# Kernel optimization log

Measured on AMD Instinct MI355X. Metric: run time of the kernel, lower is better.

## Reference

```python
import jax, jax.numpy as jnp
import numpy as np

N = 100000   # nodes
E = 1600000  # edges (avg degree 16)
D = 256      # in_channels == dim (forward hard-codes BatchNorm1d(256))
BN_EPS = 1e-5


def _batchnorm(x, gamma, beta):
    # training-mode BatchNorm1d: batch statistics over node dim, biased variance
    mu = jnp.mean(x, axis=0)
    var = jnp.var(x, axis=0)
    return (x - mu) * jax.lax.rsqrt(var + BN_EPS) * gamma + beta


def _gin_conv(x, src, dst, n, W1, b1, gamma, beta, W2, b2):
    # GINConv, eps=0: nn((1+eps)*x + sum_{j in N(i)} x_j)
    agg = jax.ops.segment_sum(x[src], dst, num_segments=n)  # sparse neighbor sum
    h = x + agg
    h = jax.nn.relu(_batchnorm(h @ W1 + b1, gamma, beta))
    return jax.nn.relu(h @ W2 + b2)


def setup_inputs() -> dict:
    key = jax.random.key(0)
    ks = jax.random.split(key, 8)
    x = jax.random.normal(ks[0], (N, D), dtype=jnp.float32)
    edge_index = jax.random.randint(ks[1], (2, E), 0, N, dtype=jnp.int64)
    s = 0.02
    inp = {
        "x": x,
        "edge_index": edge_index,
        # fresh BatchNorm1d(256) in forward (default affine params)
        "g0": jnp.ones((D,), jnp.float32),
        "b0": jnp.zeros((D,), jnp.float32),
        # conv1 MLP: Linear-BN-ReLU-Linear-ReLU
        "W1a": jax.random.normal(ks[2], (D, D), jnp.float32) * s,
        "b1a": jnp.zeros((D,), jnp.float32),
        "g1": jnp.ones((D,), jnp.float32),
        "bt1": jnp.zeros((D,), jnp.float32),
        "W1b": jax.random.normal(ks[3], (D, D), jnp.float32) * s,
        "b1b": jnp.zeros((D,), jnp.float32),
        # conv2 MLP
        "W2a": jax.random.normal(ks[4], (D, D), jnp.float32) * s,
        "b2a": jnp.zeros((D,), jnp.float32),
        "g2": jnp.ones((D,), jnp.float32),
        "bt2": jnp.zeros((D,), jnp.float32),
        "W2b": jax.random.normal(ks[5], (D, D), jnp.float32) * s,
        "b2b": jnp.zeros((D,), jnp.float32),
    }
    return inp


def reference(x, edge_index, g0, b0, W1a, b1a, g1, bt1, W1b, b1b,
              W2a, b2a, g2, bt2, W2b, b2b):
    n = x.shape[0]
    src, dst = edge_index[0], edge_index[1]
    h = _batchnorm(x, g0, b0)                       # fresh BN(256) on input
    h = _gin_conv(h, src, dst, n, W1a, b1a, g1, bt1, W1b, b1b)
    h = jax.nn.relu(h)                              # outer relu (dropout=eval, identity)
    h = _gin_conv(h, src, dst, n, W2a, b2a, g2, bt2, W2b, b2b)
    return jax.nn.relu(h)
```

## Files before the change

kernel.cpp:

```cpp
#include <hip/hip_runtime.h>

#define N_NODES 100000
#define N_EDGES 1600000
#define DIM 256
#define NBINS 196
#define BINCAP 16384

typedef unsigned short bf16u;
typedef __attribute__((ext_vector_type(8))) short bf16x8s;
typedef __attribute__((ext_vector_type(4))) float f32x4;

__device__ __forceinline__ float bf2f(unsigned int u16) {
    union { unsigned int i; float f; } x; x.i = u16 << 16; return x.f;
}
__device__ __forceinline__ float hi2f(unsigned int u) {
    union { unsigned int i; float f; } x; x.i = u & 0xffff0000u; return x.f;
}
__device__ __forceinline__ float lo2f(unsigned int u) {
    union { unsigned int i; float f; } x; x.i = u << 16; return x.f;
}
__device__ __forceinline__ bf16u f2bf(float f) {
    union { float f; unsigned int i; } x; x.f = f;
    unsigned int i = x.i;
    return (bf16u)((i + 0x7fffu + ((i >> 16) & 1u)) >> 16);
}
__device__ __forceinline__ float loadv(const void* p, size_t i, int isf32) {
    return isf32 ? ((const float*)p)[i] : bf2f(((const bf16u*)p)[i]);
}
__device__ __forceinline__ void async_copy16(const void* g, void* l) {
    __builtin_amdgcn_global_load_lds((const __attribute__((address_space(1))) void*)g,
                                     (__attribute__((address_space(3))) void*)l, 16, 0, 0);
}

__global__ void zero_floats(float* p, int n) {
    int i = blockIdx.x * 256 + threadIdx.x;
    if (i < n) p[i] = 0.f;
}

__global__ void detect_flags(const unsigned* xw, const int* ei, int* flags, int* gBinFill) {
    __shared__ int cnt, nz;
    if (threadIdx.x == 0) { cnt = 0; nz = 0; }
    __syncthreads();
    gBinFill[threadIdx.x] = 0;
    unsigned u = xw[threadIdx.x];
    float av = fabsf(bf2f(u & 0xffffu));
    if (av > 1e-5f && av < 50.f) atomicAdd(&cnt, 1);
    if (ei[2 * threadIdx.x + 1] != 0) atomicAdd(&nz, 1);
    __syncthreads();
    if (threadIdx.x == 0) {
        flags[0] = (cnt >= 128) ? 0 : 1;
        if (nz == 0) { flags[1] = 2; flags[2] = 2 * N_EDGES; }
        else         { flags[1] = 1; flags[2] = N_EDGES; }
    }
}

__global__ void transpose_w(const void* W0, const void* W1, const void* W2, const void* W3,
                            bf16u* Wt, const int* flags) {
    __shared__ bf16u tile[64][65];
    int isf32 = flags[0];
    const void* W = (blockIdx.y == 0) ? W0 : (blockIdx.y == 1) ? W1 : (blockIdx.y == 2) ? W2 : W3;
    bf16u* out = Wt + (size_t)blockIdx.y * DIM * DIM;
    int t = threadIdx.x;
    int tx = t & 63, ty = t >> 6;
    int k0 = (blockIdx.x >> 2) * 64, n0 = (blockIdx.x & 3) * 64;
#pragma unroll
    for (int i = 0; i < 16; ++i) {
        int r = ty + i * 4;
        tile[tx][r] = f2bf(loadv(W, (size_t)(k0 + r) * DIM + (n0 + tx), isf32));
    }
    __syncthreads();
#pragma unroll
    for (int i = 0; i < 16; ++i) {
        int r = ty + i * 4;
        out[(size_t)(n0 + r) * DIM + (k0 + tx)] = tile[r][tx];
    }
}

__global__ __launch_bounds__(256) void bin_scatter(const int* __restrict__ ei,
                                                   const int* __restrict__ flags,
                                                   uint2* __restrict__ gRec,
                                                   int* __restrict__ gBinFill) {
    __shared__ int cnt[256];
    __shared__ int cur[256];
    __shared__ uint2 rec[4096];
    int t = threadIdx.x;
    cnt[t] = 0; cur[t] = 0;
    __syncthreads();
    int st = flags[1], ofs = flags[2];
    int e0 = blockIdx.x * 4096;
#pragma unroll
    for (int i = 0; i < 16; ++i) {
        int e = e0 + i * 256 + t;
        uint2 r;
        if (e < N_EDGES) {
            r.x = (unsigned)ei[(size_t)ofs + (size_t)e * st];
            r.y = (unsigned)ei[(size_t)e * st];
            atomicAdd(&cnt[r.x >> 9], 1);
        } else {
            r.x = 0xffffffffu; r.y = 0;
        }
        rec[i * 256 + t] = r;
    }
    __syncthreads();
    if (t < NBINS) {
        int c = cnt[t];
        int b = (c > 0) ? atomicAdd(&gBinFill[t], c) : 0;
        cnt[t] = b;
    }
    __syncthreads();
#pragma unroll
    for (int i = 0; i < 16; ++i) {
        uint2 r = rec[i * 256 + t];
        if (r.x != 0xffffffffu) {
            int b = r.x >> 9;
            int li = atomicAdd(&cur[b], 1);
            int pos = cnt[b] + li;
            if (pos < BINCAP) gRec[(size_t)b * BINCAP + pos] = r;
        }
    }
}

__global__ void bin_scan(const int* gBinFill, int* binBase) {
    __shared__ int s[256];
    int t = threadIdx.x;
    s[t] = (t < NBINS) ? gBinFill[t] : 0;
    __syncthreads();
    for (int off = 1; off < 256; off <<= 1) {
        int v = (t >= off) ? s[t - off] : 0;
        __syncthreads();
        s[t] += v;
        __syncthreads();
    }
    binBase[t + 1] = s[t];
    if (t == 0) binBase[0] = 0;
}

__global__ __launch_bounds__(256) void bin_csr(const uint2* __restrict__ gRec,
                                               const int* __restrict__ gBinFill,
                                               const int* __restrict__ binBase,
                                               int* __restrict__ rp, int* __restrict__ col) {
    __shared__ int cntA[512], scanB[512], noff[512], ncur[512];
    int bin = blockIdx.x, t = threadIdx.x;
    int cnt = gBinFill[bin];
    if (cnt > BINCAP) cnt = BINCAP;
    int gbase = binBase[bin], lo = bin << 9;
    cntA[t] = 0; cntA[t + 256] = 0; ncur[t] = 0; ncur[t + 256] = 0;
    __syncthreads();
    const uint2* R = gRec + (size_t)bin * BINCAP;
    for (int j = t; j < cnt; j += 256) atomicAdd(&cntA[(int)R[j].x - lo], 1);
    __syncthreads();
    scanB[t] = cntA[t]; scanB[t + 256] = cntA[t + 256];
    __syncthreads();
    for (int off = 1; off < 512; off <<= 1) {
        int v0 = (t >= off) ? scanB[t - off] : 0;
        int v1 = (t + 256 >= off) ? scanB[t + 256 - off] : 0;
        __syncthreads();
        scanB[t] += v0; scanB[t + 256] += v1;
        __syncthreads();
    }
    noff[t] = scanB[t] - cntA[t];
    noff[t + 256] = scanB[t + 256] - cntA[t + 256];
    __syncthreads();
    int n0 = lo + t, n1 = lo + t + 256;
    if (n0 < N_NODES) rp[n0] = gbase + noff[t];
    if (n1 < N_NODES) rp[n1] = gbase + noff[t + 256];
    if (bin == 0 && t == 0) rp[N_NODES] = N_EDGES;
    for (int j = t; j < cnt; j += 256) {
        uint2 r = R[j];
        int k = (int)r.x - lo;
        int li = atomicAdd(&ncur[k], 1);
        col[gbase + noff[k] + li] = (int)r.y;
    }
}

__global__ void col_stats(const void* X, int nrows, float* sums, const int* flags, int dual) {
    __shared__ float ls[512];
    int isf32 = dual ? flags[0] : 0;
    int t = threadIdx.x;
    ls[t] = 0.f; ls[t + 256] = 0.f;
    __syncthreads();
    int rpb = (nrows + gridDim.x - 1) / gridDim.x;
    int r0 = blockIdx.x * rpb;
    int r1 = r0 + rpb; if (r1 > nrows) r1 = nrows;
    int cg = (t & 31) * 8;
    float s[8], q[8];
#pragma unroll
    for (int j = 0; j < 8; ++j) { s[j] = 0.f; q[j] = 0.f; }
    for (int r = r0 + (t >> 5); r < r1; r += 8) {
        size_t base = (size_t)r * DIM + cg;
#pragma unroll
        for (int j = 0; j < 8; ++j) {
            float f = loadv(X, base + j, isf32);
            s[j] += f; q[j] += f * f;
        }
    }
#pragma unroll
    for (int j = 0; j < 8; ++j) {
        atomicAdd(&ls[cg + j], s[j]);
        atomicAdd(&ls[256 + cg + j], q[j]);
    }
    __syncthreads();
    atomicAdd(&sums[t], ls[t]);
    atomicAdd(&sums[256 + t], ls[256 + t]);
}

__global__ void bn_finalize(const float* sums, const void* gamma, const void* beta,
                            float* sc, float* sh, float inv_n, const int* flags) {
    int isf32 = flags[0];
    int t = threadIdx.x;
    float mu = sums[t] * inv_n;
    float var = sums[256 + t] * inv_n - mu * mu;
    float rs = rsqrtf(var + 1e-5f);
    float g = loadv(gamma, t, isf32), b = loadv(beta, t, isf32);
    sc[t] = rs * g;
    sh[t] = b - mu * rs * g;
}

__global__ void bn_apply(const void* X, const float* sc, const float* sh, bf16u* Y,
                         const int* flags, int dual, int relu) {
    int isf32 = dual ? flags[0] : 0;
    size_t i = (size_t)blockIdx.x * 256 + threadIdx.x;
    int c = ((int)(i & 31)) * 8;
    size_t base = i * 8;
    float v[8];
    if (isf32) {
        f32x4 x0 = *(const f32x4*)((const float*)X + base);
        f32x4 x1 = *(const f32x4*)((const float*)X + base + 4);
#pragma unroll
        for (int j = 0; j < 4; ++j) { v[j] = x0[j]; v[4 + j] = x1[j]; }
    } else {
        uint4 u = *(const uint4*)((const bf16u*)X + base);
        v[0] = lo2f(u.x); v[1] = hi2f(u.x);
        v[2] = lo2f(u.y); v[3] = hi2f(u.y);
        v[4] = lo2f(u.z); v[5] = hi2f(u.z);
        v[6] = lo2f(u.w); v[7] = hi2f(u.w);
    }
    f32x4 s0 = *(const f32x4*)(sc + c), s1 = *(const f32x4*)(sc + c + 4);
    f32x4 h0 = *(const f32x4*)(sh + c), h1 = *(const f32x4*)(sh + c + 4);
    float y[8];
#pragma unroll
    for (int j = 0; j < 4; ++j) {
        y[j]     = v[j]     * s0[j] + h0[j];
        y[4 + j] = v[4 + j] * s1[j] + h1[j];
    }
    if (relu) {
#pragma unroll
        for (int j = 0; j < 8; ++j) y[j] = fmaxf(y[j], 0.f);
    }
    uint4 ov;
    ov.x = (unsigned)f2bf(y[0]) | ((unsigned)f2bf(y[1]) << 16);
    ov.y = (unsigned)f2bf(y[2]) | ((unsigned)f2bf(y[3]) << 16);
    ov.z = (unsigned)f2bf(y[4]) | ((unsigned)f2bf(y[5]) << 16);
    ov.w = (unsigned)f2bf(y[6]) | ((unsigned)f2bf(y[7]) << 16);
    *(uint4*)(Y + base) = ov;
}

__global__ __launch_bounds__(256) void aggregate(const bf16u* __restrict__ h,
                                                 const int* __restrict__ rp,
                                                 const int* __restrict__ col,
                                                 bf16u* __restrict__ out) {
    int node = blockIdx.x * 4 + (threadIdx.x >> 6);
    int lane = threadIdx.x & 63;
    int p = lane >> 5, c = lane & 31;
    const uint4* hv = (const uint4*)h;
    float acc[8];
    if (p == 0) {
        uint4 u = hv[(size_t)node * 32 + c];
        acc[0] = lo2f(u.x); acc[1] = hi2f(u.x);
        acc[2] = lo2f(u.y); acc[3] = hi2f(u.y);
        acc[4] = lo2f(u.z); acc[5] = hi2f(u.z);
        acc[6] = lo2f(u.w); acc[7] = hi2f(u.w);
    } else {
#pragma unroll
        for (int j = 0; j < 8; ++j) acc[j] = 0.f;
    }
    int e = rp[node], e1 = rp[node + 1];
    for (; e + 4 <= e1; e += 4) {
        int s0 = col[e + p];
        int s1 = col[e + 2 + p];
        uint4 a = hv[(size_t)s0 * 32 + c];
        uint4 b = hv[(size_t)s1 * 32 + c];
        acc[0] += lo2f(a.x); acc[1] += hi2f(a.x);
        acc[2] += lo2f(a.y); acc[3] += hi2f(a.y);
        acc[4] += lo2f(a.z); acc[5] += hi2f(a.z);
        acc[6] += lo2f(a.w); acc[7] += hi2f(a.w);
        acc[0] += lo2f(b.x); acc[1] += hi2f(b.x);
        acc[2] += lo2f(b.y); acc[3] += hi2f(b.y);
        acc[4] += lo2f(b.z); acc[5] += hi2f(b.z);
        acc[6] += lo2f(b.w); acc[7] += hi2f(b.w);
    }
    for (; e < e1; e += 2) {
        int idx = e + p;
        if (idx < e1) {
            uint4 a = hv[(size_t)col[idx] * 32 + c];
            acc[0] += lo2f(a.x); acc[1] += hi2f(a.x);
            acc[2] += lo2f(a.y); acc[3] += hi2f(a.y);
            acc[4] += lo2f(a.z); acc[5] += hi2f(a.z);
            acc[6] += lo2f(a.w); acc[7] += hi2f(a.w);
        }
    }
#pragma unroll
    for (int j = 0; j < 8; ++j) acc[j] += __shfl_xor(acc[j], 32);
    if (p == 0) {
        uint4 ov;
        ov.x = (unsigned)f2bf(acc[0]) | ((unsigned)f2bf(acc[1]) << 16);
        ov.y = (unsigned)f2bf(acc[2]) | ((unsigned)f2bf(acc[3]) << 16);
        ov.z = (unsigned)f2bf(acc[4]) | ((unsigned)f2bf(acc[5]) << 16);
        ov.w = (unsigned)f2bf(acc[6]) | ((unsigned)f2bf(acc[7]) << 16);
        ((uint4*)out)[(size_t)node * 32 + c] = ov;
    }
}

__global__ __launch_bounds__(256) void gemm_bias(const bf16u* __restrict__ A,
                                                 const bf16u* __restrict__ Wt,
                                                 const void* __restrict__ bias,
                                                 void* __restrict__ Cout, int mrows,
                                                 const int* __restrict__ flags,
                                                 int relu, int f32out,
                                                 float* __restrict__ stats) {
    __shared__ bf16u As[128 * 64];
    __shared__ bf16u Bs[128 * 64];
    __shared__ float lsum[256];
    int isf32 = flags[0];
    int t = threadIdx.x;
    int w = t >> 6, lane = t & 63;
    int lr = lane & 15, lq = lane >> 4;
    int wm = w >> 1, wn = w & 1;
    int rowBase = blockIdx.x * 128, colBase = blockIdx.y * 128;
    f32x4 acc[4][4] = {};
    lsum[t] = 0.f;
    int srow = t >> 3;
    int g8   = ((t & 7) ^ ((t >> 3) & 7)) * 8;
    for (int k0 = 0; k0 < 256; k0 += 64) {
        __syncthreads();
#pragma unroll
        for (int p = 0; p < 4; ++p) {
            int r = p * 32 + srow;
            int gr = rowBase + r; gr = (gr < mrows) ? gr : (mrows - 1);
            async_copy16(A + (size_t)gr * 256 + k0 + g8, &As[(p * 32 + (w << 3)) * 64]);
            async_copy16(Wt + (size_t)(colBase + r) * 256 + k0 + g8, &Bs[(p * 32 + (w << 3)) * 64]);
        }
        __syncthreads();
#pragma unroll
        for (int ks = 0; ks < 2; ++ks) {
            bf16x8s af[4], bfv[4];
#pragma unroll
            for (int mt = 0; mt < 4; ++mt) {
                int ar = wm * 64 + mt * 16 + lr;
                af[mt] = *(const bf16x8s*)&As[ar * 64 + (((ks * 4 + lq) ^ (lr & 7)) * 8)];
            }
#pragma unroll
            for (int nt = 0; nt < 4; ++nt) {
                int br = wn * 64 + nt * 16 + lr;
                bfv[nt] = *(const bf16x8s*)&Bs[br * 64 + (((ks * 4 + lq) ^ (lr & 7)) * 8)];
            }
#pragma unroll
            for (int mt = 0; mt < 4; ++mt)
#pragma unroll
                for (int nt = 0; nt < 4; ++nt)
                    acc[mt][nt] = __builtin_amdgcn_mfma_f32_16x16x32_bf16(af[mt], bfv[nt], acc[mt][nt], 0, 0, 0);
        }
    }
    int storef32 = f32out && isf32;
#pragma unroll
    for (int nt = 0; nt < 4; ++nt) {
        int cl = wn * 64 + nt * 16 + lr;
        int c = colBase + cl;
        float bv = loadv(bias, c, isf32);
        float ssum = 0.f, ssq = 0.f;
#pragma unroll
        for (int mt = 0; mt < 4; ++mt) {
            int r0 = rowBase + wm * 64 + mt * 16 + lq * 4;
#pragma unroll
            for (int j = 0; j < 4; ++j) {
                int r = r0 + j;
                if (r < mrows) {
                    float y = acc[mt][nt][j] + bv;
                    if (relu) y = fmaxf(y, 0.f);
                    if (storef32) ((float*)Cout)[(size_t)r * 256 + c] = y;
                    else          ((bf16u*)Cout)[(size_t)r * 256 + c] = f2bf(y);
                    ssum += y; ssq += y * y;
                }
            }
        }
        if (stats) {
            atomicAdd(&lsum[cl], ssum);
            atomicAdd(&lsum[128 + cl], ssq);
        }
    }
    if (stats) {
        __syncthreads();
        if (t < 128) {
            atomicAdd(&stats[colBase + t], lsum[t]);
            atomicAdd(&stats[256 + colBase + t], lsum[128 + t]);
        }
    }
}

extern "C" void kernel_launch(void* const* d_in, const int* in_sizes, int n_in,
                              void* d_out, int out_size, void* d_ws, size_t ws_size,
                              hipStream_t stream) {
    const void* x   = d_in[0];
    const int*  ei  = (const int*)d_in[1];
    const void* g0  = d_in[2];
    const void* b0  = d_in[3];
    const void* W1a = d_in[4];
    const void* b1a = d_in[5];
    const void* g1  = d_in[6];
    const void* bt1 = d_in[7];
    const void* W1b = d_in[8];
    const void* b1b = d_in[9];
    const void* W2a = d_in[10];
    const void* b2a = d_in[11];
    const void* g2  = d_in[12];
    const void* bt2 = d_in[13];
    const void* W2b = d_in[14];
    const void* b2b = d_in[15];

    char* ws = (char*)d_ws;
    size_t off = 0;
    auto alloc = [&](size_t bytes) {
        char* p = ws + off;
        off += (bytes + 255) & ~(size_t)255;
        return p;
    };
    const size_t FB = (size_t)N_NODES * DIM * 2;
    bf16u* bufA  = (bf16u*)alloc(FB);
    bf16u* bufB  = (bf16u*)alloc(FB);
    bf16u* Wt    = (bf16u*)alloc((size_t)4 * DIM * DIM * 2);
    int*   colA  = (int*)alloc((size_t)N_EDGES * 4);
    int*   rp    = (int*)alloc((size_t)(N_NODES + 1) * 4);
    int*   gBinFill = (int*)alloc(256 * 4);
    int*   binBase  = (int*)alloc(260 * 4);
    float* sums0 = (float*)alloc(512 * 4);
    float* sums1 = (float*)alloc(512 * 4);
    float* sums2 = (float*)alloc(512 * 4);
    float* sc    = (float*)alloc(256 * 4);
    float* sh    = (float*)alloc(256 * 4);
    int*   flags = (int*)alloc(4 * 4);

    uint2* gRec = (uint2*)bufB;

    bf16u* Wt1a = Wt;
    bf16u* Wt1b = Wt + 65536;
    bf16u* Wt2a = Wt + 2 * 65536;
    bf16u* Wt2b = Wt + 3 * 65536;

    const float inv_n = 1.0f / (float)N_NODES;

    detect_flags<<<1, 256, 0, stream>>>((const unsigned*)x, ei, flags, gBinFill);
    zero_floats<<<6, 256, 0, stream>>>(sums0, 1536);
    transpose_w<<<dim3(16, 4), 256, 0, stream>>>(W1a, W1b, W2a, W2b, Wt, flags);

    bin_scatter<<<391, 256, 0, stream>>>(ei, flags, gRec, gBinFill);
    bin_scan<<<1, 256, 0, stream>>>(gBinFill, binBase);
    bin_csr<<<NBINS, 256, 0, stream>>>(gRec, gBinFill, binBase, rp, colA);

    col_stats<<<500, 256, 0, stream>>>(x, N_NODES, sums0, flags, 1);
    bn_finalize<<<1, 256, 0, stream>>>(sums0, g0, b0, sc, sh, inv_n, flags);
    bn_apply<<<12500, 256, 0, stream>>>(x, sc, sh, bufB, flags, 1, 0);

    aggregate<<<25000, 256, 0, stream>>>(bufB, rp, colA, bufA);
    gemm_bias<<<dim3(782, 2), 256, 0, stream>>>(bufA, Wt1a, b1a, bufB, N_NODES, flags, 0, 0, sums1);
    bn_finalize<<<1, 256, 0, stream>>>(sums1, g1, bt1, sc, sh, inv_n, flags);
    bn_apply<<<12500, 256, 0, stream>>>(bufB, sc, sh, bufB, flags, 0, 1);
    gemm_bias<<<dim3(782, 2), 256, 0, stream>>>(bufB, Wt1b, b1b, bufA, N_NODES, flags, 1, 0, nullptr);

    aggregate<<<25000, 256, 0, stream>>>(bufA, rp, colA, bufB);
    gemm_bias<<<dim3(782, 2), 256, 0, stream>>>(bufB, Wt2a, b2a, bufA, N_NODES, flags, 0, 0, sums2);
    bn_finalize<<<1, 256, 0, stream>>>(sums2, g2, bt2, sc, sh, inv_n, flags);
    bn_apply<<<12500, 256, 0, stream>>>(bufA, sc, sh, bufA, flags, 0, 1);
    gemm_bias<<<dim3(782, 2), 256, 0, stream>>>(bufA, Wt2b, b2b, d_out, N_NODES, flags, 1, 1, nullptr);
}
```

Before: 855.9 us.

## Fuse BN-apply+ReLU into GEMM A-load, remap GEMM blocks per XCD, misc tweaks

The second GEMM of each GIN MLP now applies the BatchNorm scale/shift and ReLU while staging A into LDS, which removes two separate bn_apply passes over the 100k x 256 activation. GEMM blocks are remapped so that consecutive work tiles land on the same XCD, which should improve L2 reuse. Other changes: the stats zeroing moves into detect_flags, col_stats gets a vectorized f32 load path, and the aggregate loop is unrolled to 8 edges. The fused path replaces the async LDS copy with a synchronous register load and conversion, which can reduce load/compute overlap in the GEMM.

After: 824.8 us. 1.04x faster.

```diff
diff --git a/kernel.cpp b/kernel.cpp
--- a/kernel.cpp
+++ b/kernel.cpp
@@ -32,16 +32,14 @@
                                      (__attribute__((address_space(3))) void*)l, 16, 0, 0);
 }
 
-__global__ void zero_floats(float* p, int n) {
-    int i = blockIdx.x * 256 + threadIdx.x;
-    if (i < n) p[i] = 0.f;
-}
-
-__global__ void detect_flags(const unsigned* xw, const int* ei, int* flags, int* gBinFill) {
+__global__ void detect_flags(const unsigned* xw, const int* ei, int* flags, int* gBinFill,
+                             float* sums) {
     __shared__ int cnt, nz;
     if (threadIdx.x == 0) { cnt = 0; nz = 0; }
     __syncthreads();
     gBinFill[threadIdx.x] = 0;
+#pragma unroll
+    for (int i = 0; i < 6; ++i) sums[i * 256 + threadIdx.x] = 0.f;
     unsigned u = xw[threadIdx.x];
     float av = fabsf(bf2f(u & 0xffffu));
     if (av > 1e-5f && av < 50.f) atomicAdd(&cnt, 1);
@@ -186,12 +184,24 @@
     float s[8], q[8];
 #pragma unroll
     for (int j = 0; j < 8; ++j) { s[j] = 0.f; q[j] = 0.f; }
-    for (int r = r0 + (t >> 5); r < r1; r += 8) {
-        size_t base = (size_t)r * DIM + cg;
-#pragma unroll
-        for (int j = 0; j < 8; ++j) {
-            float f = loadv(X, base + j, isf32);
-            s[j] += f; q[j] += f * f;
+    if (isf32) {
+        for (int r = r0 + (t >> 5); r < r1; r += 8) {
+            const float* xp = (const float*)X + (size_t)r * DIM + cg;
+            f32x4 a = *(const f32x4*)xp, b = *(const f32x4*)(xp + 4);
+#pragma unroll
+            for (int j = 0; j < 4; ++j) {
+                s[j] += a[j]; q[j] += a[j] * a[j];
+                s[4 + j] += b[j]; q[4 + j] += b[j] * b[j];
+            }
+        }
+    } else {
+        for (int r = r0 + (t >> 5); r < r1; r += 8) {
+            size_t base = (size_t)r * DIM + cg;
+#pragma unroll
+            for (int j = 0; j < 8; ++j) {
+                float f = bf2f(((const bf16u*)X)[base + j]);
+                s[j] += f; q[j] += f * f;
+            }
         }
     }
 #pragma unroll
@@ -275,28 +285,36 @@
         for (int j = 0; j < 8; ++j) acc[j] = 0.f;
     }
     int e = rp[node], e1 = rp[node + 1];
-    for (; e + 4 <= e1; e += 4) {
-        int s0 = col[e + p];
-        int s1 = col[e + 2 + p];
+    for (; e + 8 <= e1; e += 8) {
+        int s0 = col[e + p], s1 = col[e + 2 + p], s2 = col[e + 4 + p], s3 = col[e + 6 + p];
         uint4 a = hv[(size_t)s0 * 32 + c];
         uint4 b = hv[(size_t)s1 * 32 + c];
-        acc[0] += lo2f(a.x); acc[1] += hi2f(a.x);
-        acc[2] += lo2f(a.y); acc[3] += hi2f(a.y);
-        acc[4] += lo2f(a.z); acc[5] += hi2f(a.z);
-        acc[6] += lo2f(a.w); acc[7] += hi2f(a.w);
-        acc[0] += lo2f(b.x); acc[1] += hi2f(b.x);
-        acc[2] += lo2f(b.y); acc[3] += hi2f(b.y);
-        acc[4] += lo2f(b.z); acc[5] += hi2f(b.z);
-        acc[6] += lo2f(b.w); acc[7] += hi2f(b.w);
+        uint4 d = hv[(size_t)s2 * 32 + c];
+        uint4 f = hv[(size_t)s3 * 32 + c];
+        acc[0] += lo2f(a.x); acc[1] += hi2f(a.x); acc[2] += lo2f(a.y); acc[3] += hi2f(a.y);
+        acc[4] += lo2f(a.z); acc[5] += hi2f(a.z); acc[6] += lo2f(a.w); acc[7] += hi2f(a.w);
+        acc[0] += lo2f(b.x); acc[1] += hi2f(b.x); acc[2] += lo2f(b.y); acc[3] += hi2f(b.y);
+        acc[4] += lo2f(b.z); acc[5] += hi2f(b.z); acc[6] += lo2f(b.w); acc[7] += hi2f(b.w);
+        acc[0] += lo2f(d.x); acc[1] += hi2f(d.x); acc[2] += lo2f(d.y); acc[3] += hi2f(d.y);
+        acc[4] += lo2f(d.z); acc[5] += hi2f(d.z); acc[6] += lo2f(d.w); acc[7] += hi2f(d.w);
+        acc[0] += lo2f(f.x); acc[1] += hi2f(f.x); acc[2] += lo2f(f.y); acc[3] += hi2f(f.y);
+        acc[4] += lo2f(f.z); acc[5] += hi2f(f.z); acc[6] += lo2f(f.w); acc[7] += hi2f(f.w);
+    }
+    for (; e + 4 <= e1; e += 4) {
+        int s0 = col[e + p], s1 = col[e + 2 + p];
+        uint4 a = hv[(size_t)s0 * 32 + c];
+        uint4 b = hv[(size_t)s1 * 32 + c];
+        acc[0] += lo2f(a.x); acc[1] += hi2f(a.x); acc[2] += lo2f(a.y); acc[3] += hi2f(a.y);
+        acc[4] += lo2f(a.z); acc[5] += hi2f(a.z); acc[6] += lo2f(a.w); acc[7] += hi2f(a.w);
+        acc[0] += lo2f(b.x); acc[1] += hi2f(b.x); acc[2] += lo2f(b.y); acc[3] += hi2f(b.y);
+        acc[4] += lo2f(b.z); acc[5] += hi2f(b.z); acc[6] += lo2f(b.w); acc[7] += hi2f(b.w);
     }
     for (; e < e1; e += 2) {
         int idx = e + p;
         if (idx < e1) {
             uint4 a = hv[(size_t)col[idx] * 32 + c];
-            acc[0] += lo2f(a.x); acc[1] += hi2f(a.x);
-            acc[2] += lo2f(a.y); acc[3] += hi2f(a.y);
-            acc[4] += lo2f(a.z); acc[5] += hi2f(a.z);
-            acc[6] += lo2f(a.w); acc[7] += hi2f(a.w);
+            acc[0] += lo2f(a.x); acc[1] += hi2f(a.x); acc[2] += lo2f(a.y); acc[3] += hi2f(a.y);
+            acc[4] += lo2f(a.z); acc[5] += hi2f(a.z); acc[6] += lo2f(a.w); acc[7] += hi2f(a.w);
         }
     }
 #pragma unroll
@@ -317,7 +335,9 @@
                                                  void* __restrict__ Cout, int mrows,
                                                  const int* __restrict__ flags,
                                                  int relu, int f32out,
-                                                 float* __restrict__ stats) {
+                                                 float* __restrict__ stats,
+                                                 const float* __restrict__ bnsc,
+                                                 const float* __restrict__ bnsh) {
     __shared__ bf16u As[128 * 64];
     __shared__ bf16u Bs[128 * 64];
     __shared__ float lsum[256];
@@ -326,19 +346,51 @@
     int w = t >> 6, lane = t & 63;
     int lr = lane & 15, lq = lane >> 4;
     int wm = w >> 1, wn = w & 1;
-    int rowBase = blockIdx.x * 128, colBase = blockIdx.y * 128;
+    int xcd = blockIdx.x & 7, j0 = blockIdx.x >> 3;
+    int wkid = ((xcd < 4) ? xcd * 196 : 784 + (xcd - 4) * 195) + j0;
+    int rowBase = (wkid >> 1) * 128, colBase = (wkid & 1) * 128;
     f32x4 acc[4][4] = {};
     lsum[t] = 0.f;
     int srow = t >> 3;
     int g8   = ((t & 7) ^ ((t >> 3) & 7)) * 8;
     for (int k0 = 0; k0 < 256; k0 += 64) {
         __syncthreads();
-#pragma unroll
-        for (int p = 0; p < 4; ++p) {
-            int r = p * 32 + srow;
-            int gr = rowBase + r; gr = (gr < mrows) ? gr : (mrows - 1);
-            async_copy16(A + (size_t)gr * 256 + k0 + g8, &As[(p * 32 + (w << 3)) * 64]);
-            async_copy16(Wt + (size_t)(colBase + r) * 256 + k0 + g8, &Bs[(p * 32 + (w << 3)) * 64]);
+        if (bnsc) {
+            f32x4 s0v = *(const f32x4*)(bnsc + k0 + g8);
+            f32x4 s1v = *(const f32x4*)(bnsc + k0 + g8 + 4);
+            f32x4 h0v = *(const f32x4*)(bnsh + k0 + g8);
+            f32x4 h1v = *(const f32x4*)(bnsh + k0 + g8 + 4);
+#pragma unroll
+            for (int p = 0; p < 4; ++p) {
+                int r = p * 32 + srow;
+                int gr = rowBase + r; gr = (gr < mrows) ? gr : (mrows - 1);
+                uint4 av = *(const uint4*)(A + (size_t)gr * 256 + k0 + g8);
+                float y0 = fmaxf(lo2f(av.x) * s0v[0] + h0v[0], 0.f);
+                float y1 = fmaxf(hi2f(av.x) * s0v[1] + h0v[1], 0.f);
+                float y2 = fmaxf(lo2f(av.y) * s0v[2] + h0v[2], 0.f);
+                float y3 = fmaxf(hi2f(av.y) * s0v[3] + h0v[3], 0.f);
+                float y4 = fmaxf(lo2f(av.z) * s1v[0] + h1v[0], 0.f);
+                float y5 = fmaxf(hi2f(av.z) * s1v[1] + h1v[1], 0.f);
+                float y6 = fmaxf(lo2f(av.w) * s1v[2] + h1v[2], 0.f);
+                float y7 = fmaxf(hi2f(av.w) * s1v[3] + h1v[3], 0.f);
+                uint4 ov;
+                ov.x = (unsigned)f2bf(y0) | ((unsigned)f2bf(y1) << 16);
+                ov.y = (unsigned)f2bf(y2) | ((unsigned)f2bf(y3) << 16);
+                ov.z = (unsigned)f2bf(y4) | ((unsigned)f2bf(y5) << 16);
+                ov.w = (unsigned)f2bf(y6) | ((unsigned)f2bf(y7) << 16);
+                *(uint4*)&As[r * 64 + (t & 7) * 8] = ov;
+                async_copy16(Wt + (size_t)(colBase + r) * 256 + k0 + g8,
+                             &Bs[(p * 32 + (w << 3)) * 64]);
+            }
+        } else {
+#pragma unroll
+            for (int p = 0; p < 4; ++p) {
+                int r = p * 32 + srow;
+                int gr = rowBase + r; gr = (gr < mrows) ? gr : (mrows - 1);
+                async_copy16(A + (size_t)gr * 256 + k0 + g8, &As[(p * 32 + (w << 3)) * 64]);
+                async_copy16(Wt + (size_t)(colBase + r) * 256 + k0 + g8,
+                             &Bs[(p * 32 + (w << 3)) * 64]);
+            }
         }
         __syncthreads();
 #pragma unroll
@@ -448,8 +500,7 @@
 
     const float inv_n = 1.0f / (float)N_NODES;
 
-    detect_flags<<<1, 256, 0, stream>>>((const unsigned*)x, ei, flags, gBinFill);
-    zero_floats<<<6, 256, 0, stream>>>(sums0, 1536);
+    detect_flags<<<1, 256, 0, stream>>>((const unsigned*)x, ei, flags, gBinFill, sums0);
     transpose_w<<<dim3(16, 4), 256, 0, stream>>>(W1a, W1b, W2a, W2b, Wt, flags);
 
     bin_scatter<<<391, 256, 0, stream>>>(ei, flags, gRec, gBinFill);
@@ -461,14 +512,16 @@
     bn_apply<<<12500, 256, 0, stream>>>(x, sc, sh, bufB, flags, 1, 0);
 
     aggregate<<<25000, 256, 0, stream>>>(bufB, rp, colA, bufA);
-    gemm_bias<<<dim3(782, 2), 256, 0, stream>>>(bufA, Wt1a, b1a, bufB, N_NODES, flags, 0, 0, sums1);
+    gemm_bias<<<1564, 256, 0, stream>>>(bufA, Wt1a, b1a, bufB, N_NODES, flags, 0, 0, sums1,
+                                        nullptr, nullptr);
     bn_finalize<<<1, 256, 0, stream>>>(sums1, g1, bt1, sc, sh, inv_n, flags);
-    bn_apply<<<12500, 256, 0, stream>>>(bufB, sc, sh, bufB, flags, 0, 1);
-    gemm_bias<<<dim3(782, 2), 256, 0, stream>>>(bufB, Wt1b, b1b, bufA, N_NODES, flags, 1, 0, nullptr);
+    gemm_bias<<<1564, 256, 0, stream>>>(bufB, Wt1b, b1b, bufA, N_NODES, flags, 1, 0, nullptr,
+                                        sc, sh);
 
     aggregate<<<25000, 256, 0, stream>>>(bufA, rp, colA, bufB);
-    gemm_bias<<<dim3(782, 2), 256, 0, stream>>>(bufB, Wt2a, b2a, bufA, N_NODES, flags, 0, 0, sums2);
+    gemm_bias<<<1564, 256, 0, stream>>>(bufB, Wt2a, b2a, bufA, N_NODES, flags, 0, 0, sums2,
+                                        nullptr, nullptr);
     bn_finalize<<<1, 256, 0, stream>>>(sums2, g2, bt2, sc, sh, inv_n, flags);
-    bn_apply<<<12500, 256, 0, stream>>>(bufA, sc, sh, bufA, flags, 0, 1);
-    gemm_bias<<<dim3(782, 2), 256, 0, stream>>>(bufA, Wt2b, b2b, d_out, N_NODES, flags, 1, 1, nullptr);
-}
+    gemm_bias<<<1564, 256, 0, stream>>>(bufA, Wt2b, b2b, d_out, N_NODES, flags, 1, 1, nullptr,
+                                        sc, sh);
+}
```
